# Optimization experiments

Measured on AMD Instinct MI355X. Metric: run time of the kernel, lower is better.

## Reference

```python
import jax, jax.numpy as jnp
import numpy as np

S, B, C = 7, 2, 20
EPS = 1e-6
LAMBDA_COORD = 5.0
LAMBDA_NOOBJ = 0.5


def setup_inputs() -> dict:
    key = jax.random.key(0)
    k1, k2 = jax.random.split(key)
    N = 16384
    p = jax.random.uniform(k1, (N, S, S, B * 5 + C), dtype=jnp.float32)
    a = jax.random.uniform(k2, (N, S, S, B * 5 + C), dtype=jnp.float32)
    return {"p": p, "a": a}


def _attr(t, i):
    # i-th attribute of each of the B boxes: channels C+i, C+i+5, ... -> [N,S,S,B]
    return t[..., C + i::5]


def _coords(t):
    x, y, w, h = _attr(t, 0), _attr(t, 1), _attr(t, 2), _attr(t, 3)
    tl = jnp.stack((x - w / 2.0, y - h / 2.0), axis=-1)  # [N,S,S,B,2]
    br = jnp.stack((x + w / 2.0, y + h / 2.0), axis=-1)
    return tl, br


def _sse(x, y):
    return jnp.sum((x - y) ** 2)


def reference(p, a):
    # pairwise IoU between predicted boxes (axis 3) and target boxes (axis 4)
    p_tl, p_br = _coords(p)
    a_tl, a_br = _coords(a)
    tl = jnp.maximum(p_tl[:, :, :, :, None, :], a_tl[:, :, :, None, :, :])  # [N,S,S,B,B,2]
    br = jnp.minimum(p_br[:, :, :, :, None, :], a_br[:, :, :, None, :, :])
    sides = jnp.clip(br - tl, 0.0)
    inter = sides[..., 0] * sides[..., 1]  # [N,S,S,B,B]
    p_area = (_attr(p, 2) * _attr(p, 3))[:, :, :, :, None]
    a_area = (_attr(a, 2) * _attr(a, 3))[:, :, :, None, :]
    union = p_area + a_area - inter
    zero_union = union == 0.0
    iou = jnp.where(zero_union, 0.0, inter) / jnp.where(zero_union, EPS, union)
    max_iou = jnp.max(iou, axis=-1)  # [N,S,S,B]

    obj_i = (_attr(a, 4) > 0.0)[..., 0:1]  # [N,S,S,1]
    responsible = jnp.argmax(max_iou, axis=-1, keepdims=True) == jnp.arange(B)  # [N,S,S,B]
    obj_ij = (obj_i & responsible).astype(p.dtype)
    noobj_ij = 1.0 - obj_ij

    loss_x = _sse(obj_ij * _attr(a, 0), obj_ij * _attr(p, 0))
    loss_y = _sse(obj_ij * _attr(a, 1), obj_ij * _attr(p, 1))
    loss_w = _sse(obj_ij * jnp.sign(_attr(a, 2)) * jnp.sqrt(_attr(a, 2) + EPS),
                  obj_ij * jnp.sign(_attr(p, 2)) * jnp.sqrt(_attr(p, 2) + EPS))
    loss_h = _sse(obj_ij * jnp.sign(_attr(a, 3)) * jnp.sqrt(_attr(a, 3) + EPS),
                  obj_ij * jnp.sign(_attr(p, 3)) * jnp.sqrt(_attr(p, 3) + EPS))
    loss_conf_obj = _sse(obj_ij * obj_ij, obj_ij * _attr(p, 4))
    loss_conf_noobj = _sse(noobj_ij * obj_ij, noobj_ij * _attr(p, 4))
    obj_if = obj_i.astype(p.dtype)
    cls_loss = _sse(obj_if * p[..., 5 * B:], obj_if * a[..., 5 * B:])

    return (LAMBDA_COORD * (loss_x + loss_y + loss_w + loss_h)
            + loss_conf_obj + LAMBDA_NOOBJ * loss_conf_noobj + cls_loss)
```

## Files before the change

kernel.cpp:

```cpp
#include <hip/hip_runtime.h>


#define CH      30
#define EPSL    1e-6f
#define TPB     128
#define TILE_F  (TPB * CH)
#define TILE_F4 (TILE_F / 4)
#define BUF_F   (2 * TILE_F)
#define GRID    512

typedef const __attribute__((address_space(1))) void* gas_ptr;
typedef __attribute__((address_space(3))) void* las_ptr;

__device__ __forceinline__ float sgnf(float x) {
    return (x > 0.0f) ? 1.0f : ((x < 0.0f) ? -1.0f : 0.0f);
}

__device__ __forceinline__ void stage_tile(const float* __restrict__ p,
                                           const float* __restrict__ a,
                                           float* buf, long long tile,
                                           int wid, int lane) {
    const float* gp = p + tile * (long long)TILE_F;
    const float* ga = a + tile * (long long)TILE_F;
#pragma unroll
    for (int k = 0; k < 8; ++k) {
        const int b4 = k * TPB + wid * 64;
        if (b4 < TILE_F4) {
            __builtin_amdgcn_global_load_lds(
                (gas_ptr)(gp + (size_t)(b4 + lane) * 4),
                (las_ptr)(buf + (size_t)b4 * 4), 16, 0, 0);
        }
    }
#pragma unroll
    for (int k = 0; k < 8; ++k) {
        const int b4 = k * TPB + wid * 64;
        if (b4 < TILE_F4) {
            __builtin_amdgcn_global_load_lds(
                (gas_ptr)(ga + (size_t)(b4 + lane) * 4),
                (las_ptr)(buf + TILE_F + (size_t)b4 * 4), 16, 0, 0);
        }
    }
}

__device__ __forceinline__ float cell_loss(const float* pd, const float* ad) {
    float lsum = 0.0f;

    float pxv[2], pyv[2], pwv[2], phv[2], pcv[2];
    float axv[2], ayv[2], awv[2], ahv[2];
#pragma unroll
    for (int b = 0; b < 2; ++b) {
        pxv[b] = pd[10 + 5 * b]; pyv[b] = pd[11 + 5 * b];
        pwv[b] = pd[12 + 5 * b]; phv[b] = pd[13 + 5 * b];
        pcv[b] = pd[14 + 5 * b];
        axv[b] = ad[10 + 5 * b]; ayv[b] = ad[11 + 5 * b];
        awv[b] = ad[12 + 5 * b]; ahv[b] = ad[13 + 5 * b];
    }
    const bool obj = ad[14] > 0.0f;

    float miou[2];
#pragma unroll
    for (int pb = 0; pb < 2; ++pb) {
        const float p_tlx = pxv[pb] - 0.5f * pwv[pb];
        const float p_tly = pyv[pb] - 0.5f * phv[pb];
        const float p_brx = pxv[pb] + 0.5f * pwv[pb];
        const float p_bry = pyv[pb] + 0.5f * phv[pb];
        const float p_area = pwv[pb] * phv[pb];
        float best = -3.4e38f;
#pragma unroll
        for (int ab = 0; ab < 2; ++ab) {
            const float a_tlx = axv[ab] - 0.5f * awv[ab];
            const float a_tly = ayv[ab] - 0.5f * ahv[ab];
            const float a_brx = axv[ab] + 0.5f * awv[ab];
            const float a_bry = ayv[ab] + 0.5f * ahv[ab];
            float sx = fminf(p_brx, a_brx) - fmaxf(p_tlx, a_tlx);
            float sy = fminf(p_bry, a_bry) - fmaxf(p_tly, a_tly);
            sx = fmaxf(sx, 0.0f);
            sy = fmaxf(sy, 0.0f);
            const float inter = sx * sy;
            const float uni = p_area + awv[ab] * ahv[ab] - inter;
            const float iou = (uni == 0.0f) ? 0.0f : (inter / uni);
            best = fmaxf(best, iou);
        }
        miou[pb] = best;
    }
    const int resp = (miou[1] > miou[0]) ? 1 : 0;

#pragma unroll
    for (int b = 0; b < 2; ++b) {
        const bool oij = obj && (b == resp);
        if (oij) {
            const float dx = axv[b] - pxv[b];
            const float dy = ayv[b] - pyv[b];
            const float dw = sgnf(awv[b]) * sqrtf(awv[b] + EPSL) - sgnf(pwv[b]) * sqrtf(pwv[b] + EPSL);
            const float dh = sgnf(ahv[b]) * sqrtf(ahv[b] + EPSL) - sgnf(phv[b]) * sqrtf(phv[b] + EPSL);
            const float dc = 1.0f - pcv[b];
            lsum += 5.0f * (dx * dx + dy * dy + dw * dw + dh * dh) + dc * dc;
        } else {
            lsum += 0.5f * pcv[b] * pcv[b];
        }
    }

    if (obj) {
#pragma unroll
        for (int k = 0; k < 20; ++k) {
            const float d = pd[k] - ad[k];
            lsum += d * d;
        }
    }
    return lsum;
}

__global__ __launch_bounds__(TPB) void yolo_loss_kernel(const float* __restrict__ p,
                                                        const float* __restrict__ a,
                                                        float* __restrict__ out,
                                                        long long n_cells) {
    __shared__ float lds[2][BUF_F];
    __shared__ float wsum[TPB / 64];

    const int tid  = threadIdx.x;
    const int wid  = tid >> 6;
    const int lane = tid & 63;
    const long long FT = n_cells / TPB;
    const int nb = gridDim.x;

    float lsum = 0.0f;
    long long t = blockIdx.x;
    int cur = 0;

    if (t < FT) stage_tile(p, a, lds[0], t, wid, lane);
    __syncthreads();

    for (; t < FT; t += nb) {
        const long long tn = t + nb;
        if (tn < FT) stage_tile(p, a, lds[cur ^ 1], tn, wid, lane);

        float pd[20], ad[20];
        const float* bp = lds[cur] + tid * CH + 10;
        const float* ba = lds[cur] + TILE_F + tid * CH + 10;
#pragma unroll
        for (int i = 0; i < 10; ++i) {
            const float2 v = *(const float2*)(bp + 2 * i);
            pd[2 * i] = v.x; pd[2 * i + 1] = v.y;
        }
#pragma unroll
        for (int i = 0; i < 10; ++i) {
            const float2 v = *(const float2*)(ba + 2 * i);
            ad[2 * i] = v.x; ad[2 * i + 1] = v.y;
        }
        lsum += cell_loss(pd, ad);

        __syncthreads();
        cur ^= 1;
    }

    if (blockIdx.x == 0) {
        const long long c = FT * TPB + tid;
        if (c < n_cells) {
            float pd[20], ad[20];
            const float2* cp2 = (const float2*)(p + c * CH + 10);
            const float2* ca2 = (const float2*)(a + c * CH + 10);
#pragma unroll
            for (int i = 0; i < 10; ++i) {
                const float2 v = cp2[i];
                pd[2 * i] = v.x; pd[2 * i + 1] = v.y;
            }
#pragma unroll
            for (int i = 0; i < 10; ++i) {
                const float2 v = ca2[i];
                ad[2 * i] = v.x; ad[2 * i + 1] = v.y;
            }
            lsum += cell_loss(pd, ad);
        }
    }

    float v = lsum;
#pragma unroll
    for (int off = 32; off > 0; off >>= 1)
        v += __shfl_down(v, off, 64);
    if ((tid & 63) == 0) wsum[tid >> 6] = v;
    __syncthreads();
    if (tid == 0) {
        float t2 = 0.0f;
#pragma unroll
        for (int w = 0; w < TPB / 64; ++w) t2 += wsum[w];
        atomicAdd(out, t2);
    }
}

extern "C" void kernel_launch(void* const* d_in, const int* in_sizes, int n_in,
                              void* d_out, int out_size, void* d_ws, size_t ws_size,
                              hipStream_t stream) {
    const float* p = (const float*)d_in[0];
    const float* a = (const float*)d_in[1];
    float* out = (float*)d_out;

    const long long n_cells = (long long)in_sizes[0] / CH;

    hipMemsetAsync(d_out, 0, sizeof(float), stream);
    yolo_loss_kernel<<<GRID, TPB, 0, stream>>>(p, a, out, n_cells);
}
```

Baseline: 211.6 us.

## Replace LDS-direct async loads with register-prefetch staging and contiguous tile ranges

Removes the global_load_lds double-buffered staging. Each thread now prefetches the next tile into float4 registers, then writes them to a single LDS buffer after a barrier. Each block is given a contiguous range of tiles instead of a grid-stride walk, and the grid grows from 512 to 1280 blocks. This trades the direct-to-LDS DMA path for more vector registers and an extra barrier per tile, in exchange for more blocks in flight and sequential access within each block.

```diff
diff --git a/kernel.cpp b/kernel.cpp
--- a/kernel.cpp
+++ b/kernel.cpp
@@ -4,42 +4,14 @@
 #define CH      30
 #define EPSL    1e-6f
 #define TPB     128
-#define TILE_F  (TPB * CH)
+#define TILE_C  128
+#define TILE_F  (TILE_C * CH)
 #define TILE_F4 (TILE_F / 4)
-#define BUF_F   (2 * TILE_F)
-#define GRID    512
-
-typedef const __attribute__((address_space(1))) void* gas_ptr;
-typedef __attribute__((address_space(3))) void* las_ptr;
+#define NLOAD   8
+#define GRID    1280
 
 __device__ __forceinline__ float sgnf(float x) {
     return (x > 0.0f) ? 1.0f : ((x < 0.0f) ? -1.0f : 0.0f);
-}
-
-__device__ __forceinline__ void stage_tile(const float* __restrict__ p,
-                                           const float* __restrict__ a,
-                                           float* buf, long long tile,
-                                           int wid, int lane) {
-    const float* gp = p + tile * (long long)TILE_F;
-    const float* ga = a + tile * (long long)TILE_F;
-#pragma unroll
-    for (int k = 0; k < 8; ++k) {
-        const int b4 = k * TPB + wid * 64;
-        if (b4 < TILE_F4) {
-            __builtin_amdgcn_global_load_lds(
-                (gas_ptr)(gp + (size_t)(b4 + lane) * 4),
-                (las_ptr)(buf + (size_t)b4 * 4), 16, 0, 0);
-        }
-    }
-#pragma unroll
-    for (int k = 0; k < 8; ++k) {
-        const int b4 = k * TPB + wid * 64;
-        if (b4 < TILE_F4) {
-            __builtin_amdgcn_global_load_lds(
-                (gas_ptr)(ga + (size_t)(b4 + lane) * 4),
-                (las_ptr)(buf + TILE_F + (size_t)b4 * 4), 16, 0, 0);
-        }
-    }
 }
 
 __device__ __forceinline__ float cell_loss(const float* pd, const float* ad) {
@@ -114,47 +86,85 @@
                                                         const float* __restrict__ a,
                                                         float* __restrict__ out,
                                                         long long n_cells) {
-    __shared__ float lds[2][BUF_F];
+    __shared__ float buf[2 * TILE_F];
     __shared__ float wsum[TPB / 64];
 
-    const int tid  = threadIdx.x;
-    const int wid  = tid >> 6;
-    const int lane = tid & 63;
-    const long long FT = n_cells / TPB;
-    const int nb = gridDim.x;
+    const int tid = threadIdx.x;
+    const long long FT = n_cells / TILE_C;
+    const long long nb = gridDim.x;
+    const long long b  = blockIdx.x;
+    const long long q = FT / nb, r = FT % nb;
+    const long long start = b * q + (b < r ? b : r);
+    const long long end   = start + q + (b < r ? 1 : 0);
 
     float lsum = 0.0f;
-    long long t = blockIdx.x;
-    int cur = 0;
-
-    if (t < FT) stage_tile(p, a, lds[0], t, wid, lane);
+    float4 rp[NLOAD], ra[NLOAD];
+
+    long long t = start;
+    if (t < end) {
+        const float4* gp = (const float4*)(p + t * (long long)TILE_F);
+        const float4* ga = (const float4*)(a + t * (long long)TILE_F);
+#pragma unroll
+        for (int i = 0; i < NLOAD; ++i) {
+            const int idx = i * TPB + tid;
+            if (idx < TILE_F4) { rp[i] = gp[idx]; ra[i] = ga[idx]; }
+        }
+#pragma unroll
+        for (int i = 0; i < NLOAD; ++i) {
+            const int idx = i * TPB + tid;
+            if (idx < TILE_F4) {
+                *(float4*)(buf + (size_t)idx * 4)          = rp[i];
+                *(float4*)(buf + TILE_F + (size_t)idx * 4) = ra[i];
+            }
+        }
+    }
     __syncthreads();
 
-    for (; t < FT; t += nb) {
-        const long long tn = t + nb;
-        if (tn < FT) stage_tile(p, a, lds[cur ^ 1], tn, wid, lane);
-
-        float pd[20], ad[20];
-        const float* bp = lds[cur] + tid * CH + 10;
-        const float* ba = lds[cur] + TILE_F + tid * CH + 10;
-#pragma unroll
-        for (int i = 0; i < 10; ++i) {
-            const float2 v = *(const float2*)(bp + 2 * i);
-            pd[2 * i] = v.x; pd[2 * i + 1] = v.y;
-        }
-#pragma unroll
-        for (int i = 0; i < 10; ++i) {
-            const float2 v = *(const float2*)(ba + 2 * i);
-            ad[2 * i] = v.x; ad[2 * i + 1] = v.y;
-        }
-        lsum += cell_loss(pd, ad);
+    for (; t < end; ++t) {
+        const long long tn = t + 1;
+        if (tn < end) {
+            const float4* gp = (const float4*)(p + tn * (long long)TILE_F);
+            const float4* ga = (const float4*)(a + tn * (long long)TILE_F);
+#pragma unroll
+            for (int i = 0; i < NLOAD; ++i) {
+                const int idx = i * TPB + tid;
+                if (idx < TILE_F4) { rp[i] = gp[idx]; ra[i] = ga[idx]; }
+            }
+        }
+
+        {
+            float pd[20], ad[20];
+            const float* bp = buf + tid * CH + 10;
+            const float* ba = buf + TILE_F + tid * CH + 10;
+#pragma unroll
+            for (int i = 0; i < 10; ++i) {
+                const float2 v = *(const float2*)(bp + 2 * i);
+                pd[2 * i] = v.x; pd[2 * i + 1] = v.y;
+            }
+#pragma unroll
+            for (int i = 0; i < 10; ++i) {
+                const float2 v = *(const float2*)(ba + 2 * i);
+                ad[2 * i] = v.x; ad[2 * i + 1] = v.y;
+            }
+            lsum += cell_loss(pd, ad);
+        }
 
         __syncthreads();
-        cur ^= 1;
+        if (tn < end) {
+#pragma unroll
+            for (int i = 0; i < NLOAD; ++i) {
+                const int idx = i * TPB + tid;
+                if (idx < TILE_F4) {
+                    *(float4*)(buf + (size_t)idx * 4)          = rp[i];
+                    *(float4*)(buf + TILE_F + (size_t)idx * 4) = ra[i];
+                }
+            }
+        }
+        __syncthreads();
     }
 
     if (blockIdx.x == 0) {
-        const long long c = FT * TPB + tid;
+        const long long c = FT * TILE_C + tid;
         if (c < n_cells) {
             float pd[20], ad[20];
             const float2* cp2 = (const float2*)(p + c * CH + 10);
```

Measured after the change: 255.6 us. +20.8%, slower.
